# Kernel optimization log

Measured on AMD Instinct MI355X. Metric: run time of the kernel, lower is better.

## Reference

```python
import jax, jax.numpy as jnp
import numpy as np
import math

N_NODES, CHANNELS, N_ELEM, N_FEAT = 4096, 128, 10, 128
LS_IN = [0, 1, 2]          # input irreps per channel: 0e+1o+2e -> dim 9
L_OUT = [0, 1]             # keep_irrep_out = {0e, 1o}
L12_MAX = 3                # cap on intermediate coupling
SLICES = {0: (0, 1), 1: (1, 4), 2: (4, 9)}
PATHS1 = [l for l in L_OUT if l in LS_IN]
PATHS2 = [(l1, l2, lo) for l1 in LS_IN for l2 in LS_IN for lo in L_OUT if abs(l1 - l2) <= lo <= l1 + l2]
T12_KEYS = [(l1, l2, l12) for l1 in LS_IN for l2 in LS_IN for l12 in range(abs(l1 - l2), min(l1 + l2, L12_MAX) + 1)]
PATHS3 = [(k, l3, lo) for k in T12_KEYS for l3 in LS_IN for lo in L_OUT if abs(k[2] - l3) <= lo <= k[2] + l3]

def _su2_cg(j1, m1, j2, m2, j3, m3):
    if m3 != m1 + m2:
        return 0.0
    f = math.factorial
    vmin = max(-j1 + j2 + m3, -j1 + m1, 0)
    vmax = min(j2 + j3 + m1, j3 - j1 + j2, j3 + m3)
    C = math.sqrt((2 * j3 + 1) * f(j3 + j1 - j2) * f(j3 - j1 + j2) * f(j1 + j2 - j3) * f(j3 + m3) * f(j3 - m3)
                  / (f(j1 + j2 + j3 + 1) * f(j1 - m1) * f(j1 + m1) * f(j2 - m2) * f(j2 + m2)))
    S = 0.0
    for v in range(vmin, vmax + 1):
        S += (-1) ** (v + j2 + m2) * f(j2 + j3 + m1 - v) * f(j1 - m1 + v) / (
            f(v) * f(j3 - j1 + j2 - v) * f(j3 + m3 - v) * f(v + j1 - j2 - m3))
    return C * S

def _c2r(l):
    # change of basis real -> complex spherical harmonics (e3nn convention)
    q = np.zeros((2 * l + 1, 2 * l + 1), dtype=np.complex128)
    for m in range(-l, 0):
        q[l + m, l + abs(m)] = 1.0 / math.sqrt(2)
        q[l + m, l - abs(m)] = -1j / math.sqrt(2)
    q[l, l] = 1.0
    for m in range(1, l + 1):
        q[l + m, l + abs(m)] = (-1) ** m / math.sqrt(2)
        q[l + m, l - abs(m)] = 1j * (-1) ** m / math.sqrt(2)
    return (-1j) ** l * q

_CG = {}
def real_cg(l1, l2, l3):
    key = (l1, l2, l3)
    if key not in _CG:
        Cc = np.zeros((2 * l1 + 1, 2 * l2 + 1, 2 * l3 + 1), dtype=np.complex128)
        for i, m1 in enumerate(range(-l1, l1 + 1)):
            for j, m2 in enumerate(range(-l2, l2 + 1)):
                for k, m3 in enumerate(range(-l3, l3 + 1)):
                    Cc[i, j, k] = _su2_cg(l1, m1, l2, m2, l3, m3)
        R = np.einsum('ij,kl,mn,ikn->jlm', _c2r(l1), _c2r(l2), np.conj(_c2r(l3).T), Cc)
        _CG[key] = np.real(R).astype(np.float32)
    return _CG[key]

def setup_inputs():
    key = jax.random.key(0)
    k = jax.random.split(key, 8)
    node_feats = jax.random.normal(k[0], (N_NODES, CHANNELS, 9), dtype=jnp.float32)
    species = jax.random.randint(k[1], (N_NODES,), 0, N_ELEM)
    w1 = jax.random.normal(k[2], (N_ELEM, len(PATHS1), CHANNELS), dtype=jnp.float32) / math.sqrt(len(PATHS1))
    w2 = jax.random.normal(k[3], (N_ELEM, len(PATHS2), CHANNELS), dtype=jnp.float32) / math.sqrt(len(PATHS2))
    w3 = jax.random.normal(k[4], (N_ELEM, len(PATHS3), CHANNELS), dtype=jnp.float32) / math.sqrt(len(PATHS3))
    lin_w0 = jax.random.normal(k[5], (CHANNELS, N_FEAT), dtype=jnp.float32)
    lin_w1 = jax.random.normal(k[6], (CHANNELS, N_FEAT), dtype=jnp.float32)
    return {"node_feats": node_feats, "w1": w1, "w2": w2, "w3": w3,
            "lin_w0": lin_w0, "lin_w1": lin_w1, "species": species}

def reference(node_feats, w1, w2, w3, lin_w0, lin_w1, species):
    n, c = node_feats.shape[:2]
    attrs = jax.nn.one_hot(species, N_ELEM, dtype=node_feats.dtype)
    A = {l: node_feats[..., SLICES[l][0]:SLICES[l][1]] for l in LS_IN}
    # element-dependent path weights per node
    w1n = jnp.einsum('ne,epc->npc', attrs, w1)
    w2n = jnp.einsum('ne,epc->npc', attrs, w2)
    w3n = jnp.einsum('ne,epc->npc', attrs, w3)
    B = {lo: jnp.zeros((n, c, 2 * lo + 1), node_feats.dtype) for lo in L_OUT}
    # correlation order 1
    for p, lo in enumerate(PATHS1):
        B[lo] = B[lo] + w1n[:, p, :, None] * A[lo]
    for p, (l1, l2, lo) in enumerate(PATHS2):
        cg = jnp.asarray(real_cg(l1, l2, lo))
        t = jnp.einsum('ijk,nci,ncj->nck', cg, A[l1], A[l2])
        B[lo] = B[lo] + w2n[:, p, :, None] * t
    T12 = {}
    for kk in T12_KEYS:
        l1, l2, l12 = kk
        T12[kk] = jnp.einsum('ijk,nci,ncj->nck', jnp.asarray(real_cg(l1, l2, l12)), A[l1], A[l2])
    for p, (kk, l3, lo) in enumerate(PATHS3):
        cg = jnp.asarray(real_cg(kk[2], l3, lo))
        t = jnp.einsum('ijk,nci,ncj->nck', cg, T12[kk], A[l3])
        B[lo] = B[lo] + w3n[:, p, :, None] * t
    # equivariant Linear: mix channel axis into num_features per output irrep
    s = 1.0 / math.sqrt(c)
    out0 = jnp.einsum('ncm,cf->nfm', B[0], lin_w0) * s
    out1 = jnp.einsum('ncm,cf->nfm', B[1], lin_w1) * s
    return jnp.concatenate([out0, out1], axis=-1)  # [N, F, 1+3]
```

## Files before the change

### kernel.cpp

```cpp
#include <hip/hip_runtime.h>
#include <utility>


#define NN 4096
#define NC 128
#define NE 10

typedef float f4u __attribute__((ext_vector_type(4), aligned(4)));

template<typename F, int... Is>
__device__ __forceinline__ void sfor_impl(F&& f, std::integer_sequence<int, Is...>) {
  (f(std::integral_constant<int, Is>{}), ...);
}
template<int N, typename F>
__device__ __forceinline__ void sfor(F&& f) {
  sfor_impl((F&&)f, std::make_integer_sequence<int, N>{});
}

constexpr int T_L1c[19]  = {0,0,0,1,1,1,1,1,1,1,2,2,2,2,2,2,2,2,3};
constexpr int T_L2c[19]  = {0,1,2,0,1,1,1,2,2,2,0,1,1,1,2,2,2,2,2};
constexpr int T_L3c[19]  = {0,1,2,1,0,1,2,1,2,3,2,1,2,3,0,1,2,3,1};
constexpr int T_OFFc[19] = {0,1,10,35,44,53,80,125,170,245,350,375,420,495,600,625,700,825,1000};
constexpr int AOFFc[3]   = {0,1,4};

constexpr int P2U_L1c[7]  = {0,0,1,1,1,2,2};
constexpr int P2U_L2c[7]  = {0,1,1,1,2,2,2};
constexpr int P2U_LOc[7]  = {0,1,0,1,1,0,1};
constexpr int P2U_TBLc[7] = {0,1,4,5,7,14,15};
constexpr int P2U_WAc[7]  = {0,1,3,4,5,7,8};
constexpr int P2U_WBc[7]  = {-1,2,-1,-1,6,-1,-1};

constexpr int K_L1c[18]  = {0,0,0,1,1,1,1,1,1,1,2,2,2,2,2,2,2,2};
constexpr int K_L2c[18]  = {0,1,2,0,1,1,1,2,2,2,0,1,1,1,2,2,2,2};
constexpr int K_L12c[18] = {0,1,2,1,0,1,2,1,2,3,2,1,2,3,0,1,2,3};

constexpr int   TT_CANONc[18] = {0,1,2,1,4,5,6,7,8,9,2,7,8,9,14,15,16,17};
constexpr float TT_SGNc[18]   = {1,1,1,1,1,1,1,1,1,1,1,1,-1,1,1,1,1,1};
constexpr int CANONc[13] = {0,1,2,4,5,6,7,8,9,14,15,16,17};
constexpr int CONS2c[13] = {-1,3,10,-1,-1,-1,11,12,13,-1,-1,-1,-1};

constexpr int P3_STARTc[19] = {0,2,6,9,13,15,19,22,26,29,30,33,37,40,41,43,47,50,51};
constexpr int P3_L3c[51] = {
  0,1,  0,1,1,2,  1,2,2,  0,1,1,2,  0,1,  0,1,1,2,  1,2,2,  0,1,1,2,  1,2,2,
  2,  1,2,2,  0,1,1,2,  1,2,2,  2,  0,1,  0,1,1,2,  1,2,2,  2 };
constexpr int P3_LOc[51] = {
  0,1,  1,0,1,1,  1,0,1,  1,0,1,1,  0,1,  1,0,1,1,  1,0,1,  1,0,1,1,  1,0,1,
  1,  1,0,1,  1,0,1,1,  1,0,1,  1,  0,1,  1,0,1,1,  1,0,1,  1 };
constexpr int P3_TBLc[51] = {
  0,1,  3,4,5,7,  11,14,15,  3,4,5,7,  0,1,  3,4,5,7,  11,14,15,  3,4,5,7,
  11,14,15,  18,  11,14,15,  3,4,5,7,  11,14,15,  18,  0,1,  3,4,5,7,
  11,14,15,  18 };

constexpr double cfact(int n) { double r = 1.0; for (int i = 2; i <= n; ++i) r *= i; return r; }
constexpr double csqrt(double x) {
  if (x <= 0.0) return 0.0;
  double r = x > 1.0 ? x : 1.0;
  for (int i = 0; i < 64; ++i) r = 0.5 * (r + x / r);
  return r;
}
constexpr double su2cg(int j1, int m1, int j2, int m2, int j3, int m3) {
  if (m3 != m1 + m2) return 0.0;
  int vmin = -j1 + j2 + m3; if (-j1 + m1 > vmin) vmin = -j1 + m1; if (vmin < 0) vmin = 0;
  int vmax = j2 + j3 + m1; if (j3 - j1 + j2 < vmax) vmax = j3 - j1 + j2; if (j3 + m3 < vmax) vmax = j3 + m3;
  double C = csqrt((2.0 * j3 + 1.0)
                   * cfact(j3 + j1 - j2) * cfact(j3 - j1 + j2) * cfact(j1 + j2 - j3)
                   * cfact(j3 + m3) * cfact(j3 - m3)
                   / (cfact(j1 + j2 + j3 + 1) * cfact(j1 - m1) * cfact(j1 + m1)
                      * cfact(j2 - m2) * cfact(j2 + m2)));
  double S = 0.0;
  for (int v = vmin; v <= vmax; ++v) {
    double sgn = ((v + j2 + m2) & 1) ? -1.0 : 1.0;
    S += sgn * cfact(j2 + j3 + m1 - v) * cfact(j1 - m1 + v)
         / (cfact(v) * cfact(j3 - j1 + j2 - v) * cfact(j3 + m3 - v) * cfact(v + j1 - j2 - m3));
  }
  return C * S;
}

struct Cx { double re, im; };
constexpr Cx cxmul(Cx a, Cx b) { return Cx{a.re * b.re - a.im * b.im, a.re * b.im + a.im * b.re}; }
struct Row { int cnt; int col[2]; Cx v[2]; };

constexpr Row c2r_row(int l, int r) {
  Row out{0, {0, 0}, {{0, 0}, {0, 0}}};
  constexpr double is2 = 0.70710678118654752440;
  const int m = r - l;
  if (m < 0) {
    out.cnt = 2;
    out.col[0] = l - m; out.v[0] = Cx{is2, 0.0};
    out.col[1] = l + m; out.v[1] = Cx{0.0, -is2};
  } else if (m == 0) {
    out.cnt = 1; out.col[0] = l; out.v[0] = Cx{1.0, 0.0};
  } else {
    const double sgn = (m & 1) ? -1.0 : 1.0;
    out.cnt = 2;
    out.col[0] = l + m; out.v[0] = Cx{sgn * is2, 0.0};
    out.col[1] = l - m; out.v[1] = Cx{0.0, sgn * is2};
  }
  const int ph = l & 3;
  for (int a = 0; a < out.cnt; ++a) {
    Cx v = out.v[a];
    out.v[a] = (ph == 0) ? v
             : (ph == 1) ? Cx{v.im, -v.re}
             : (ph == 2) ? Cx{-v.re, -v.im}
                         : Cx{-v.im, v.re};
  }
  return out;
}

struct CGAll { float v[1105]; };
constexpr CGAll make_cg() {
  CGAll R{};
  for (int t = 0; t < 19; ++t) {
    const int l1 = T_L1c[t], l2 = T_L2c[t], l3 = T_L3c[t], off = T_OFFc[t];
    const int d1 = 2 * l1 + 1, d2 = 2 * l2 + 1, d3 = 2 * l3 + 1;
    double tmp[175] = {};
    for (int i = 0; i < d1; ++i) {
      const int m1 = i - l1;
      const Row r1 = c2r_row(l1, i);
      for (int k = 0; k < d2; ++k) {
        const int m2 = k - l2, m3 = m1 + m2;
        if (m3 < -l3 || m3 > l3) continue;
        const double cc = su2cg(l1, m1, l2, m2, l3, m3);
        if (cc == 0.0) continue;
        const Row r2 = c2r_row(l2, k);
        const Row r3 = c2r_row(l3, m3 + l3);
        for (int a = 0; a < r1.cnt; ++a)
          for (int b = 0; b < r2.cnt; ++b) {
            const Cx q12 = cxmul(r1.v[a], r2.v[b]);
            for (int cdx = 0; cdx < r3.cnt; ++cdx) {
              const double re = q12.re * r3.v[cdx].re + q12.im * r3.v[cdx].im;
              tmp[(r1.col[a] * d2 + r2.col[b]) * d3 + r3.col[cdx]] += re * cc;
            }
          }
      }
    }
    const int sz = d1 * d2 * d3;
    for (int e = 0; e < sz; ++e) R.v[off + e] = (float)tmp[e];
  }
  return R;
}
constexpr CGAll CG_ALL = make_cg();

constexpr bool check_cg_sym() {
  for (int t = 0; t < 18; ++t) {
    const int tc = TT_CANONc[t];
    if (tc == t) continue;
    const int l1 = K_L1c[t], l2 = K_L2c[t], l12 = K_L12c[t];
    const int d1 = 2*l1+1, d2 = 2*l2+1, d12 = 2*l12+1;
    for (int i = 0; i < d1; ++i)
      for (int j = 0; j < d2; ++j)
        for (int k = 0; k < d12; ++k) {
          float a = CG_ALL.v[T_OFFc[t]  + (i*d2 + j)*d12 + k];
          float b = TT_SGNc[t] * CG_ALL.v[T_OFFc[tc] + (j*d1 + i)*d12 + k];
          float d = a - b; if (d < 0) d = -d;
          if (d > 1e-5f) return false;
        }
  }
  return true;
}
static_assert(check_cg_sym(), "CG exchange symmetry violated");

__global__ __launch_bounds__(256) void epb_wt(
    const float* __restrict__ w1,
    const float* __restrict__ w2,
    const float* __restrict__ w3,
    float* __restrict__ wt)
{
  const int idx = blockIdx.x * 256 + threadIdx.x;
  const int c = idx & 127;
  const int j = (idx >> 7) & 63;
  const int e = idx >> 13;
  float v = 0.f;
  if (j < 2)       v = w1[((size_t)e * 2  + j)       * NC + c];
  else if (j < 11) v = w2[((size_t)e * 9  + (j - 2)) * NC + c];
  else if (j < 62) v = w3[((size_t)e * 51 + (j - 11)) * NC + c];
  wt[((size_t)(e * NC + c)) * 64 + j] = v;
}

__global__ __launch_bounds__(256) void epb_fused(
    const float*  __restrict__ nf,
    const float*  __restrict__ wt,
    const float4* __restrict__ lw0_4,
    const float4* __restrict__ lw1_4,
    const int*    __restrict__ species,
    float* __restrict__ out)
{
  __shared__ float4 Bsh[2 * NC];
  __shared__ float4 Red[8 * NC];

  const int t  = threadIdx.x;
  const int nb = blockIdx.x * 2;

  {
    const int nl = t >> 7;
    const int c  = t & 127;
    const int n  = nb + nl;
    const int s  = species[n];

    const float* ap = nf + ((size_t)n * NC + c) * 9;
    float A[9];
    {
      const f4u v0 = *reinterpret_cast<const f4u*>(ap);
      const f4u v1 = *reinterpret_cast<const f4u*>(ap + 4);
      sfor<4>([&](auto I) { A[I.value] = v0[I.value]; A[I.value + 4] = v1[I.value]; });
      A[8] = ap[8];
    }

    const float* wtp = wt + ((size_t)(s * NC + c)) * 64;

    float B[4];
    {
      const float wa = wtp[0], wb = wtp[1];
      B[0] = wa * A[0];
      B[1] = wb * A[1];
      B[2] = wb * A[2];
      B[3] = wb * A[3];
    }

    sfor<7>([&](auto P) {
      constexpr int p  = P.value;
      constexpr int l1 = P2U_L1c[p], l2 = P2U_L2c[p], lo = P2U_LOc[p];
      constexpr int d1 = 2*l1+1, d2 = 2*l2+1, dl = 2*lo+1;
      constexpr int off = T_OFFc[P2U_TBLc[p]];
      float w = wtp[2 + P2U_WAc[p]];
      if constexpr (P2U_WBc[p] >= 0) w += wtp[2 + P2U_WBc[p]];
      sfor<dl>([&](auto Kk) {
        constexpr int k = Kk.value;
        float v = 0.f;
        sfor<d1>([&](auto I) {
          sfor<d2>([&](auto J) {
            constexpr float cgc = CG_ALL.v[off + (I.value * d2 + J.value) * dl + k];
            if constexpr (cgc != 0.0f) {
              constexpr int ia = AOFFc[l1] + I.value, ja = AOFFc[l2] + J.value;
              constexpr int x = ia < ja ? ia : ja, y = ia < ja ? ja : ia;
              v = fmaf(cgc, A[x] * A[y], v);
            }
          });
        });
        B[lo + k] = fmaf(w, v, B[lo + k]);
      });
    });

    sfor<13>([&](auto CI) {
      constexpr int tk  = CANONc[CI.value];
      constexpr int l1  = K_L1c[tk], l2 = K_L2c[tk], l12 = K_L12c[tk];
      constexpr int d1  = 2*l1+1, d2 = 2*l2+1, d12 = 2*l12+1;
      constexpr int off = T_OFFc[tk];
      float tt[d12];
      sfor<d12>([&](auto Kk) {
        constexpr int k = Kk.value;
        float v = 0.f;
        sfor<d1>([&](auto I) {
          sfor<d2>([&](auto J) {
            constexpr float cgc = CG_ALL.v[off + (I.value * d2 + J.value) * d12 + k];
            if constexpr (cgc != 0.0f) {
              constexpr int ia = AOFFc[l1] + I.value, ja = AOFFc[l2] + J.value;
              constexpr int x = ia < ja ? ia : ja, y = ia < ja ? ja : ia;
              v = fmaf(cgc, A[x] * A[y], v);
            }
          });
        });
        tt[k] = v;
      });

      auto consume = [&](auto TK, auto SG) {
        constexpr int tkey = TK.value;
        constexpr float sgn = (float)SG.value;
        constexpr int pcnt = P3_STARTc[tkey + 1] - P3_STARTc[tkey];
        sfor<pcnt>([&](auto PP) {
          constexpr int p  = P3_STARTc[tkey] + PP.value;
          constexpr int l3 = P3_L3c[p], lo = P3_LOc[p];
          constexpr int d3 = 2*l3+1, dl = 2*lo+1;
          constexpr int off2 = T_OFFc[P3_TBLc[p]];
          const float w = wtp[11 + p];
          sfor<dl>([&](auto M) {
            float v = 0.f;
            sfor<d12>([&](auto Kk) {
              sfor<d3>([&](auto J) {
                constexpr float cgc = sgn * CG_ALL.v[off2 + (Kk.value * d3 + J.value) * dl + M.value];
                if constexpr (cgc != 0.0f)
                  v = fmaf(cgc, tt[Kk.value] * A[AOFFc[l3] + J.value], v);
              });
            });
            B[lo + M.value] = fmaf(w, v, B[lo + M.value]);
          });
        });
      };
      consume(std::integral_constant<int, tk>{}, std::integral_constant<int, 1>{});
      constexpr int td = CONS2c[CI.value];
      if constexpr (td >= 0)
        consume(std::integral_constant<int, td>{},
                std::integral_constant<int, (int)TT_SGNc[td]>{});
    });

    Bsh[nl * NC + c] = make_float4(B[0], B[1], B[2], B[3]);
  }
  __syncthreads();

  const int q   = t & 31;
  const int wv  = (t >> 5) & 3;
  const int nl2 = t >> 7;

  float4 acc[4] = {};

  const float4* w0c = lw0_4 + (size_t)(wv * 32) * 32 + q;
  const float4* w1c = lw1_4 + (size_t)(wv * 32) * 32 + q;
  const float4* bp  = &Bsh[nl2 * NC + wv * 32];

  #pragma unroll 4
  for (int i = 0; i < 32; ++i) {
    const float4 wa = w0c[i * 32];
    const float4 wb = w1c[i * 32];
    const float4 b  = bp[i];
    acc[0].x = fmaf(b.x, wa.x, acc[0].x); acc[0].y = fmaf(b.y, wb.x, acc[0].y);
    acc[0].z = fmaf(b.z, wb.x, acc[0].z); acc[0].w = fmaf(b.w, wb.x, acc[0].w);
    acc[1].x = fmaf(b.x, wa.y, acc[1].x); acc[1].y = fmaf(b.y, wb.y, acc[1].y);
    acc[1].z = fmaf(b.z, wb.y, acc[1].z); acc[1].w = fmaf(b.w, wb.y, acc[1].w);
    acc[2].x = fmaf(b.x, wa.z, acc[2].x); acc[2].y = fmaf(b.y, wb.z, acc[2].y);
    acc[2].z = fmaf(b.z, wb.z, acc[2].z); acc[2].w = fmaf(b.w, wb.z, acc[2].w);
    acc[3].x = fmaf(b.x, wa.w, acc[3].x); acc[3].y = fmaf(b.y, wb.w, acc[3].y);
    acc[3].z = fmaf(b.z, wb.w, acc[3].z); acc[3].w = fmaf(b.w, wb.w, acc[3].w);
  }

  sfor<4>([&](auto F_) {
    Red[(nl2 * 4 + F_.value) * NC + wv * 32 + q] = acc[F_.value];
  });
  __syncthreads();

  const float s4 = 0.08838834764831845f;
  float4* o4 = reinterpret_cast<float4*>(out);
  {
    const int n   = t >> 7;
    const int rem = t & 127;
    const int row = (n * 4 + (rem & 3)) * NC + (rem >> 2);
    const float4 r0 = Red[row];
    const float4 r1 = Red[row + 32];
    const float4 r2 = Red[row + 64];
    const float4 r3 = Red[row + 96];
    o4[(size_t)(nb + n) * NC + rem] = make_float4(
        ((r0.x + r1.x) + (r2.x + r3.x)) * s4,
        ((r0.y + r1.y) + (r2.y + r3.y)) * s4,
        ((r0.z + r1.z) + (r2.z + r3.z)) * s4,
        ((r0.w + r1.w) + (r2.w + r3.w)) * s4);
  }
}

extern "C" void kernel_launch(void* const* d_in, const int* in_sizes, int n_in,
                              void* d_out, int out_size, void* d_ws, size_t ws_size,
                              hipStream_t stream) {
  const float* nf  = (const float*)d_in[0];
  const float* w1  = (const float*)d_in[1];
  const float* w2  = (const float*)d_in[2];
  const float* w3  = (const float*)d_in[3];
  const float* lw0 = (const float*)d_in[4];
  const float* lw1 = (const float*)d_in[5];
  const int*   spc = (const int*)  d_in[6];
  float* out = (float*)d_out;
  float* wt  = (float*)d_ws;
  (void)ws_size; (void)in_sizes; (void)n_in; (void)out_size;

  hipLaunchKernelGGL(epb_wt, dim3(NE * NC * 64 / 256), dim3(256), 0, stream,
                     w1, w2, w3, wt);
  hipLaunchKernelGGL(epb_fused, dim3(NN / 2), dim3(256), 0, stream,
                     nf, wt, (const float4*)lw0, (const float4*)lw1,
                     spc, out);
}
```

Before: 111.5 us.

## Process two channels per thread with packed float2 FMAs and shuffle reduction

Each thread now handles two adjacent channels using 2-wide float vectors, so the CG contractions can map to packed FMA instructions and per-element weights are loaded as float2. The weight table is re-laid out so paired channels are interleaved, and each block now covers four nodes. The linear stage splits the channel sum into two halves per wave and combines them with a cross-lane shuffle, which removes the second shared-memory reduction buffer and its barrier. In exchange, register pressure roughly doubles, and there are half as many threads per node, each doing more work.

Measured after the change: 110.7 us. Within noise of the previous version (-0.7%).

```diff
diff --git a/kernel.cpp b/kernel.cpp
--- a/kernel.cpp
+++ b/kernel.cpp
@@ -6,7 +6,18 @@
 #define NC 128
 #define NE 10
 
-typedef float f4u __attribute__((ext_vector_type(4), aligned(4)));
+typedef float v2f __attribute__((ext_vector_type(2)));
+
+__device__ __forceinline__ v2f ld2(const float* p) {
+  return *reinterpret_cast<const v2f*>(p);
+}
+__device__ __forceinline__ v2f cfma(float c, v2f x, v2f a) {
+  v2f cc = {c, c};
+  return __builtin_elementwise_fma(cc, x, a);
+}
+__device__ __forceinline__ v2f vfma(v2f w, v2f x, v2f a) {
+  return __builtin_elementwise_fma(w, x, a);
+}
 
 template<typename F, int... Is>
 __device__ __forceinline__ void sfor_impl(F&& f, std::integer_sequence<int, Is...>) {
@@ -167,14 +178,16 @@
     float* __restrict__ wt)
 {
   const int idx = blockIdx.x * 256 + threadIdx.x;
-  const int c = idx & 127;
-  const int j = (idx >> 7) & 63;
-  const int e = idx >> 13;
+  const int b  = idx & 1;
+  const int j  = (idx >> 1) & 63;
+  const int cp = (idx >> 7) & 63;
+  const int e  = idx >> 13;
+  const int c  = cp * 2 + b;
   float v = 0.f;
-  if (j < 2)       v = w1[((size_t)e * 2  + j)       * NC + c];
-  else if (j < 11) v = w2[((size_t)e * 9  + (j - 2)) * NC + c];
+  if (j < 2)       v = w1[((size_t)e * 2  + j)        * NC + c];
+  else if (j < 11) v = w2[((size_t)e * 9  + (j - 2))  * NC + c];
   else if (j < 62) v = w3[((size_t)e * 51 + (j - 11)) * NC + c];
-  wt[((size_t)(e * NC + c)) * 64 + j] = v;
+  wt[idx] = v;
 }
 
 __global__ __launch_bounds__(256) void epb_fused(
@@ -185,32 +198,27 @@
     const int*    __restrict__ species,
     float* __restrict__ out)
 {
-  __shared__ float4 Bsh[2 * NC];
-  __shared__ float4 Red[8 * NC];
+  __shared__ float4 Bsh[4 * NC];
 
   const int t  = threadIdx.x;
-  const int nb = blockIdx.x * 2;
+  const int nb = blockIdx.x * 4;
 
   {
-    const int nl = t >> 7;
-    const int c  = t & 127;
+    const int nl = t >> 6;
+    const int cp = t & 63;
+    const int c0 = cp * 2;
     const int n  = nb + nl;
     const int s  = species[n];
 
-    const float* ap = nf + ((size_t)n * NC + c) * 9;
-    float A[9];
+    const float* ap = nf + ((size_t)n * NC + c0) * 9;
+    v2f A[9];
+    sfor<9>([&](auto I) { A[I.value] = v2f{ap[I.value], ap[I.value + 9]}; });
+
+    const float* wtp = wt + ((size_t)(s * 64 + cp)) * 128;
+
+    v2f B[4];
     {
-      const f4u v0 = *reinterpret_cast<const f4u*>(ap);
-      const f4u v1 = *reinterpret_cast<const f4u*>(ap + 4);
-      sfor<4>([&](auto I) { A[I.value] = v0[I.value]; A[I.value + 4] = v1[I.value]; });
-      A[8] = ap[8];
-    }
-
-    const float* wtp = wt + ((size_t)(s * NC + c)) * 64;
-
-    float B[4];
-    {
-      const float wa = wtp[0], wb = wtp[1];
+      const v2f wa = ld2(wtp + 0), wb = ld2(wtp + 2);
       B[0] = wa * A[0];
       B[1] = wb * A[1];
       B[2] = wb * A[2];
@@ -222,22 +230,22 @@
       constexpr int l1 = P2U_L1c[p], l2 = P2U_L2c[p], lo = P2U_LOc[p];
       constexpr int d1 = 2*l1+1, d2 = 2*l2+1, dl = 2*lo+1;
       constexpr int off = T_OFFc[P2U_TBLc[p]];
-      float w = wtp[2 + P2U_WAc[p]];
-      if constexpr (P2U_WBc[p] >= 0) w += wtp[2 + P2U_WBc[p]];
+      v2f w = ld2(wtp + 2 * (2 + P2U_WAc[p]));
+      if constexpr (P2U_WBc[p] >= 0) w = w + ld2(wtp + 2 * (2 + P2U_WBc[p]));
       sfor<dl>([&](auto Kk) {
         constexpr int k = Kk.value;
-        float v = 0.f;
+        v2f v = {0.f, 0.f};
         sfor<d1>([&](auto I) {
           sfor<d2>([&](auto J) {
             constexpr float cgc = CG_ALL.v[off + (I.value * d2 + J.value) * dl + k];
             if constexpr (cgc != 0.0f) {
               constexpr int ia = AOFFc[l1] + I.value, ja = AOFFc[l2] + J.value;
               constexpr int x = ia < ja ? ia : ja, y = ia < ja ? ja : ia;
-              v = fmaf(cgc, A[x] * A[y], v);
+              v = cfma(cgc, A[x] * A[y], v);
             }
           });
         });
-        B[lo + k] = fmaf(w, v, B[lo + k]);
+        B[lo + k] = vfma(w, v, B[lo + k]);
       });
     });
 
@@ -246,17 +254,17 @@
       constexpr int l1  = K_L1c[tk], l2 = K_L2c[tk], l12 = K_L12c[tk];
       constexpr int d1  = 2*l1+1, d2 = 2*l2+1, d12 = 2*l12+1;
       constexpr int off = T_OFFc[tk];
-      float tt[d12];
+      v2f tt[d12];
       sfor<d12>([&](auto Kk) {
         constexpr int k = Kk.value;
-        float v = 0.f;
+        v2f v = {0.f, 0.f};
         sfor<d1>([&](auto I) {
           sfor<d2>([&](auto J) {
             constexpr float cgc = CG_ALL.v[off + (I.value * d2 + J.value) * d12 + k];
             if constexpr (cgc != 0.0f) {
               constexpr int ia = AOFFc[l1] + I.value, ja = AOFFc[l2] + J.value;
               constexpr int x = ia < ja ? ia : ja, y = ia < ja ? ja : ia;
-              v = fmaf(cgc, A[x] * A[y], v);
+              v = cfma(cgc, A[x] * A[y], v);
             }
           });
         });
@@ -272,17 +280,17 @@
           constexpr int l3 = P3_L3c[p], lo = P3_LOc[p];
           constexpr int d3 = 2*l3+1, dl = 2*lo+1;
           constexpr int off2 = T_OFFc[P3_TBLc[p]];
-          const float w = wtp[11 + p];
+          const v2f w = ld2(wtp + 2 * (11 + p));
           sfor<dl>([&](auto M) {
-            float v = 0.f;
+            v2f v = {0.f, 0.f};
             sfor<d12>([&](auto Kk) {
               sfor<d3>([&](auto J) {
                 constexpr float cgc = sgn * CG_ALL.v[off2 + (Kk.value * d3 + J.value) * dl + M.value];
                 if constexpr (cgc != 0.0f)
-                  v = fmaf(cgc, tt[Kk.value] * A[AOFFc[l3] + J.value], v);
+                  v = cfma(cgc, tt[Kk.value] * A[AOFFc[l3] + J.value], v);
               });
             });
-            B[lo + M.value] = fmaf(w, v, B[lo + M.value]);
+            B[lo + M.value] = vfma(w, v, B[lo + M.value]);
           });
         });
       };
@@ -293,22 +301,24 @@
                 std::integral_constant<int, (int)TT_SGNc[td]>{});
     });
 
-    Bsh[nl * NC + c] = make_float4(B[0], B[1], B[2], B[3]);
+    Bsh[nl * NC + c0]     = make_float4(B[0].x, B[1].x, B[2].x, B[3].x);
+    Bsh[nl * NC + c0 + 1] = make_float4(B[0].y, B[1].y, B[2].y, B[3].y);
   }
   __syncthreads();
 
-  const int q   = t & 31;
-  const int wv  = (t >> 5) & 3;
-  const int nl2 = t >> 7;
+  const int nl2 = t >> 6;
+  const int ln  = t & 63;
+  const int q   = ln & 31;
+  const int h   = ln >> 5;
 
   float4 acc[4] = {};
 
-  const float4* w0c = lw0_4 + (size_t)(wv * 32) * 32 + q;
-  const float4* w1c = lw1_4 + (size_t)(wv * 32) * 32 + q;
-  const float4* bp  = &Bsh[nl2 * NC + wv * 32];
+  const float4* w0c = lw0_4 + (size_t)(h * 64) * 32 + q;
+  const float4* w1c = lw1_4 + (size_t)(h * 64) * 32 + q;
+  const float4* bp  = &Bsh[nl2 * NC + h * 64];
 
   #pragma unroll 4
-  for (int i = 0; i < 32; ++i) {
+  for (int i = 0; i < 64; ++i) {
     const float4 wa = w0c[i * 32];
     const float4 wb = w1c[i * 32];
     const float4 b  = bp[i];
@@ -323,25 +333,20 @@
   }
 
   sfor<4>([&](auto F_) {
-    Red[(nl2 * 4 + F_.value) * NC + wv * 32 + q] = acc[F_.value];
+    constexpr int f = F_.value;
+    acc[f].x += __shfl_xor(acc[f].x, 32);
+    acc[f].y += __shfl_xor(acc[f].y, 32);
+    acc[f].z += __shfl_xor(acc[f].z, 32);
+    acc[f].w += __shfl_xor(acc[f].w, 32);
   });
-  __syncthreads();
-
-  const float s4 = 0.08838834764831845f;
-  float4* o4 = reinterpret_cast<float4*>(out);
-  {
-    const int n   = t >> 7;
-    const int rem = t & 127;
-    const int row = (n * 4 + (rem & 3)) * NC + (rem >> 2);
-    const float4 r0 = Red[row];
-    const float4 r1 = Red[row + 32];
-    const float4 r2 = Red[row + 64];
-    const float4 r3 = Red[row + 96];
-    o4[(size_t)(nb + n) * NC + rem] = make_float4(
-        ((r0.x + r1.x) + (r2.x + r3.x)) * s4,
-        ((r0.y + r1.y) + (r2.y + r3.y)) * s4,
-        ((r0.z + r1.z) + (r2.z + r3.z)) * s4,
-        ((r0.w + r1.w) + (r2.w + r3.w)) * s4);
+
+  if (h == 0) {
+    const float s4 = 0.08838834764831845f;
+    float4* o4 = reinterpret_cast<float4*>(out) + (size_t)(nb + nl2) * NC + 4 * q;
+    o4[0] = make_float4(acc[0].x*s4, acc[0].y*s4, acc[0].z*s4, acc[0].w*s4);
+    o4[1] = make_float4(acc[1].x*s4, acc[1].y*s4, acc[1].z*s4, acc[1].w*s4);
+    o4[2] = make_float4(acc[2].x*s4, acc[2].y*s4, acc[2].z*s4, acc[2].w*s4);
+    o4[3] = make_float4(acc[3].x*s4, acc[3].y*s4, acc[3].z*s4, acc[3].w*s4);
   }
 }
 
@@ -361,7 +366,7 @@
 
   hipLaunchKernelGGL(epb_wt, dim3(NE * NC * 64 / 256), dim3(256), 0, stream,
                      w1, w2, w3, wt);
-  hipLaunchKernelGGL(epb_fused, dim3(NN / 2), dim3(256), 0, stream,
+  hipLaunchKernelGGL(epb_fused, dim3(NN / 4), dim3(256), 0, stream,
                      nf, wt, (const float4*)lw0, (const float4*)lw1,
                      spc, out);
 }
```
